# Optimization experiments

Hardware: AMD Instinct MI355X
Metric: run time of the kernel (lower is better)

Reference implementation:

```python
import jax, jax.numpy as jnp
import numpy as np

N = 50000        # nodes
E = 800000       # edges per meta-path (avg degree 16)
M = 3            # meta-paths
IN = 256         # in_size
HID = 16         # hidden_size (per-head out dim of GATConv)
HEADS = 8
OUT = 8          # out_size (classes)
SA_HID = 128     # StructureAttention hidden_size default
NEG_SLOPE = 0.2  # DGL GATConv leaky_relu default


def setup_inputs() -> dict:
    key = jax.random.key(0)
    ks = jax.random.split(key, 11)
    h = jax.random.normal(ks[0], (N, IN), jnp.float32)
    edges = jax.random.randint(ks[1], (M, 2, E), 0, N, jnp.int32)  # [M, (src,dst), E]
    s = 0.05
    fc_w = jax.random.normal(ks[2], (M, IN, HEADS * HID), jnp.float32) * s
    attn_l = jax.random.normal(ks[3], (M, HEADS, HID), jnp.float32) * s
    attn_r = jax.random.normal(ks[4], (M, HEADS, HID), jnp.float32) * s
    sa_w1 = jax.random.normal(ks[5], (HEADS * HID, SA_HID), jnp.float32) * s
    sa_b1 = jnp.zeros((SA_HID,), jnp.float32)
    sa_w2 = jax.random.normal(ks[6], (SA_HID, 1), jnp.float32) * s
    pred_w = jax.random.normal(ks[7], (HEADS * HID, OUT), jnp.float32) * s
    pred_b = jnp.zeros((OUT,), jnp.float32)
    return {"h": h, "edges": edges, "fc_w": fc_w, "attn_l": attn_l,
            "attn_r": attn_r, "sa_w1": sa_w1, "sa_b1": sa_b1, "sa_w2": sa_w2,
            "pred_w": pred_w, "pred_b": pred_b}


def _gat(h, src, dst, w, al, ar):
    # DGL GATConv, eval mode (dropout=0), activation=elu
    feat = (h @ w).reshape(N, HEADS, HID)                 # [N,H,D]
    el = jnp.einsum('nhd,hd->nh', feat, al)               # [N,H]
    er = jnp.einsum('nhd,hd->nh', feat, ar)               # [N,H]
    e = el[src] + er[dst]                                 # [E,H]
    e = jnp.where(e > 0, e, NEG_SLOPE * e)                # leaky_relu
    # edge softmax over incoming edges of each dst node
    emax = jax.ops.segment_max(e, dst, num_segments=N)    # [N,H]
    ex = jnp.exp(e - emax[dst])                           # [E,H]
    denom = jax.ops.segment_sum(ex, dst, num_segments=N)  # [N,H]
    alpha = ex / denom[dst]                               # [E,H]
    msg = feat[src] * alpha[:, :, None]                   # [E,H,D]
    out = jax.ops.segment_sum(msg, dst, num_segments=N)   # [N,H,D]
    return jax.nn.elu(out).reshape(N, HEADS * HID)        # flatten(1)


def reference(h, edges, fc_w, attn_l, attn_r, sa_w1, sa_b1, sa_w2, pred_w, pred_b):
    # per-meta-path GAT (loop over fixed small set of meta-paths)
    zs = [_gat(h, edges[i, 0], edges[i, 1], fc_w[i], attn_l[i], attn_r[i])
          for i in range(M)]
    z = jnp.stack(zs, axis=1)                             # [N, M, H*D]
    # StructureAttention exactly as in source: softmax over dim 0 (nodes)
    w = jnp.tanh(z @ sa_w1 + sa_b1) @ sa_w2               # [N, M, 1]
    beta = jax.nn.softmax(w, axis=0)                      # softmax over nodes
    fused = (beta * z).sum(0)                             # [M, H*D]
    return fused @ pred_w + pred_b                        # [M, OUT]
```

## Files before the change

### kernel.cpp

```cpp
#include <hip/hip_runtime.h>

#define N_NODES 50000
#define N_EDGES 800000
#define N_META 3
#define IN_DIM 256
#define HD 128
#define HEADS 8
#define HID 16
#define OUT_DIM 8
#define NBKT 196
#define BCAP 5120
#define TILE_E 4096
#define NUMPAD 2064
#define GEMM_BX ((N_NODES + 63) / 64)
#define ELER_BX ((N_NODES * HEADS + 255) / 256)

using bf16x8 = __attribute__((ext_vector_type(8))) short;
using f32x4  = __attribute__((ext_vector_type(4))) float;

__device__ __forceinline__ float bf2f(unsigned short u) {
  union { unsigned int i; float f; } x; x.i = ((unsigned int)u) << 16; return x.f;
}
__device__ __forceinline__ unsigned short f2bf(float f) {
  union { float f; unsigned int i; } x; x.f = f;
  unsigned int r = x.i + 0x7fffu + ((x.i >> 16) & 1u);
  return (unsigned short)(r >> 16);
}

__global__ __launch_bounds__(256)
void prep_kernel(const float* __restrict__ fcw, const float* __restrict__ w1,
                 unsigned short* __restrict__ fcwT, unsigned short* __restrict__ w1T) {
  int i = blockIdx.x * 256 + threadIdx.x;
  const int NFC = N_META * IN_DIM * HD;
  if (i < NFC) {
    int p = i / (IN_DIM * HD);
    int rem = i - p * (IN_DIM * HD);
    int k = rem / HD, n = rem - k * HD;
    fcwT[(size_t)p * HD * IN_DIM + n * IN_DIM + k] = f2bf(fcw[i]);
  } else if (i < NFC + HD * HD) {
    int j = i - NFC;
    int k = j / HD, n = j - k * HD;
    w1T[n * HD + k] = f2bf(w1[j]);
  }
}

__global__ __launch_bounds__(256)
void bin_gemm_kernel(const int* __restrict__ edges, int* __restrict__ gcur,
                     unsigned int* __restrict__ bktbuf,
                     const float* __restrict__ A,
                     const unsigned short* __restrict__ BT,
                     unsigned short* __restrict__ Cb, int nrows) {
  __shared__ char smem[15360];
  int p = blockIdx.y;
  int t = threadIdx.x;
  if (blockIdx.x < NBKT) {
    int* hist  = (int*)smem;
    int* gbase = hist + NBKT;
    int* fill  = gbase + NBKT;
    int e0 = blockIdx.x * TILE_E;
    const int* src = edges + (size_t)p * 2 * N_EDGES;
    const int* dst = src + N_EDGES;
    for (int i = t; i < NBKT; i += 256) { hist[i] = 0; fill[i] = 0; }
    __syncthreads();
    for (int i = t; i < TILE_E; i += 256) {
      int e = e0 + i;
      if (e < N_EDGES) atomicAdd(&hist[dst[e] >> 8], 1);
    }
    __syncthreads();
    for (int i = t; i < NBKT; i += 256) {
      int idx = p * NBKT + i;
      gbase[i] = hist[i] ? (idx * BCAP + atomicAdd(&gcur[idx], hist[i])) : 0;
    }
    __syncthreads();
    for (int i = t; i < TILE_E; i += 256) {
      int e = e0 + i;
      if (e < N_EDGES) {
        int d = dst[e];
        int b = d >> 8;
        int r = atomicAdd(&fill[b], 1);
        bktbuf[gbase[b] + r] = ((unsigned int)(d & 255) << 16) | (unsigned int)src[e];
      }
    }
  } else {
    unsigned short* As = (unsigned short*)smem;
    unsigned short* Bs = As + 64 * 40;
    int w = t >> 6, l = t & 63, q = l >> 4, s = l & 15;
    int row0 = (blockIdx.x - NBKT) * 64;
    const unsigned short* BTm = BT + (size_t)p * HD * IN_DIM;
    f32x4 acc[8] = {};
    for (int k0 = 0; k0 < IN_DIM; k0 += 32) {
      {
        int r = t >> 2, c = (t & 3) * 8;
        int gr = row0 + r;
        float4 a0, a1;
        if (gr < nrows) {
          a0 = *(const float4*)(A + (size_t)gr * IN_DIM + k0 + c);
          a1 = *(const float4*)(A + (size_t)gr * IN_DIM + k0 + c + 4);
        } else {
          a0 = make_float4(0.f, 0.f, 0.f, 0.f); a1 = a0;
        }
        ushort4 u0, u1;
        u0.x = f2bf(a0.x); u0.y = f2bf(a0.y); u0.z = f2bf(a0.z); u0.w = f2bf(a0.w);
        u1.x = f2bf(a1.x); u1.y = f2bf(a1.y); u1.z = f2bf(a1.z); u1.w = f2bf(a1.w);
        *(ushort4*)&As[r * 40 + c]     = u0;
        *(ushort4*)&As[r * 40 + c + 4] = u1;
      }
      {
        int n = t >> 1, c = (t & 1) * 16;
        uint4 b0 = *(const uint4*)(BTm + (size_t)n * IN_DIM + k0 + c);
        uint4 b1 = *(const uint4*)(BTm + (size_t)n * IN_DIM + k0 + c + 8);
        *(uint4*)&Bs[n * 40 + c]     = b0;
        *(uint4*)&Bs[n * 40 + c + 8] = b1;
      }
      __syncthreads();
      bf16x8 af = *(bf16x8*)&As[(w * 16 + s) * 40 + q * 8];
      #pragma unroll
      for (int f = 0; f < 8; ++f) {
        bf16x8 bf = *(bf16x8*)&Bs[(f * 16 + s) * 40 + q * 8];
        acc[f] = __builtin_amdgcn_mfma_f32_16x16x32_bf16(af, bf, acc[f], 0, 0, 0);
      }
      __syncthreads();
    }
    unsigned short* Cm = Cb + (size_t)p * N_NODES * HD;
    #pragma unroll
    for (int f = 0; f < 8; ++f) {
      #pragma unroll
      for (int r = 0; r < 4; ++r) {
        int gr = row0 + w * 16 + q * 4 + r;
        if (gr < nrows) Cm[(size_t)gr * HD + f * 16 + s] = f2bf(acc[f][r]);
      }
    }
  }
}

__global__ __launch_bounds__(256)
void sort_eler_kernel(const int* __restrict__ gcur,
                      const unsigned int* __restrict__ bktbuf,
                      int* __restrict__ offsB, int* __restrict__ offsE,
                      int* __restrict__ csr,
                      const unsigned short* __restrict__ featb3,
                      const float* __restrict__ al, const float* __restrict__ ar,
                      float* __restrict__ el3, float* __restrict__ er3) {
  __shared__ int lh[256];
  __shared__ int cur[256];
  __shared__ int wsum[4];
  int p = blockIdx.y;
  int t = threadIdx.x;
  if (blockIdx.x < NBKT) {
    int b = blockIdx.x;
    int lane = t & 63, wid = t >> 6;
    int idx = p * NBKT + b;
    int S = idx * BCAP;
    int E = S + gcur[idx];
    int node0 = b * 256;
    int nn = min(256, N_NODES - node0);
    int gi0 = p * N_NODES + node0;
    lh[t] = 0;
    __syncthreads();
    for (int i = S + t; i < E; i += 256) atomicAdd(&lh[bktbuf[i] >> 16], 1);
    __syncthreads();
    int v = lh[t];
    int s = v;
    #pragma unroll
    for (int d = 1; d < 64; d <<= 1) {
      int x = __shfl_up(s, d);
      if (lane >= d) s += x;
    }
    if (lane == 63) wsum[wid] = s;
    __syncthreads();
    int woff = 0;
    #pragma unroll
    for (int k = 0; k < 4; ++k) if (k < wid) woff += wsum[k];
    int excl = S + woff + s - v;
    if (t < nn) {
      offsB[gi0 + t] = excl;
      offsE[gi0 + t] = excl + v;
    }
    cur[t] = excl;
    __syncthreads();
    for (int i = S + t; i < E; i += 256) {
      unsigned int rec = bktbuf[i];
      int pos = atomicAdd(&cur[rec >> 16], 1);
      csr[pos] = (int)(rec & 0xffffu);
    }
  } else {
    int i = (blockIdx.x - NBKT) * 256 + t;
    if (i >= N_NODES * HEADS) return;
    int node = i >> 3, hh = i & 7;
    const unsigned short* f =
        featb3 + (size_t)p * N_NODES * HD + (size_t)node * HD + hh * HID;
    uint4 u0 = *(const uint4*)(f);
    uint4 u1 = *(const uint4*)(f + 8);
    unsigned int uu[8] = {u0.x, u0.y, u0.z, u0.w, u1.x, u1.y, u1.z, u1.w};
    const float* alm = al + p * HD + hh * HID;
    const float* arm = ar + p * HD + hh * HID;
    float sl = 0.f, sr = 0.f;
    #pragma unroll
    for (int q = 0; q < 8; ++q) {
      float v0 = __uint_as_float(uu[q] << 16);
      float v1 = __uint_as_float(uu[q] & 0xffff0000u);
      int d = q * 2;
      sl += v0 * alm[d] + v1 * alm[d + 1];
      sr += v0 * arm[d] + v1 * arm[d + 1];
    }
    el3[(size_t)p * N_NODES * HEADS + i] = sl;
    er3[(size_t)p * N_NODES * HEADS + i] = sr;
  }
}

__global__ __launch_bounds__(256)
void aggregate_kernel(const int* __restrict__ offsB3, const int* __restrict__ offsE3,
                      const int* __restrict__ csr,
                      const uint4* __restrict__ featb3_u4,
                      const float* __restrict__ el3, const float* __restrict__ er3,
                      uint4* __restrict__ zb3_u4) {
  int m = blockIdx.y;
  int node = blockIdx.x * 4 + (threadIdx.x >> 6);
  if (node >= N_NODES) return;
  const uint4* featb_u4 = featb3_u4 + (size_t)m * N_NODES * 16;
  const float* el = el3 + (size_t)m * N_NODES * HEADS;
  const float* er = er3 + (size_t)m * N_NODES * HEADS;
  uint4* z_u4 = zb3_u4 + (size_t)m * N_NODES * 16;
  int lane = threadIdx.x & 63;
  int k = lane >> 3, h = lane & 7;
  int qg = lane >> 4;
  int li = lane & 15;
  int ch = li >> 1;
  int beg = offsB3[m * N_NODES + node], end = offsE3[m * N_NODES + node];
  float erh = er[node * HEADS + h];
  float ssum = 0.f;
  float a[8] = {};
  int i = beg;
  for (; i + 8 <= end; i += 8) {
    int sl = csr[i + k];
    float e = el[sl * HEADS + h] + erh;
    e = e > 0.f ? e : 0.2f * e;
    float ev = __expf(e);
    ssum += ev;
    #pragma unroll
    for (int half = 0; half < 2; ++half) {
      int slot = half * 4 + qg;
      float wv = __shfl(ev, slot * 8 + ch);
      int sk = __shfl(sl, slot * 8);
      uint4 v = featb_u4[(size_t)sk * 16 + li];
      a[0] += wv * __uint_as_float(v.x << 16);
      a[1] += wv * __uint_as_float(v.x & 0xffff0000u);
      a[2] += wv * __uint_as_float(v.y << 16);
      a[3] += wv * __uint_as_float(v.y & 0xffff0000u);
      a[4] += wv * __uint_as_float(v.z << 16);
      a[5] += wv * __uint_as_float(v.z & 0xffff0000u);
      a[6] += wv * __uint_as_float(v.w << 16);
      a[7] += wv * __uint_as_float(v.w & 0xffff0000u);
    }
  }
  if (i < end) {
    int nk = end - i;
    int sl = 0; float ev = 0.f;
    if (k < nk) {
      sl = csr[i + k];
      float e = el[sl * HEADS + h] + erh;
      e = e > 0.f ? e : 0.2f * e;
      ev = __expf(e);
    }
    ssum += ev;
    #pragma unroll
    for (int half = 0; half < 2; ++half) {
      if (half * 4 < nk) {
        int slot = half * 4 + qg;
        float wv = __shfl(ev, slot * 8 + ch);
        int sk = __shfl(sl, slot * 8);
        uint4 v = featb_u4[(size_t)sk * 16 + li];
        a[0] += wv * __uint_as_float(v.x << 16);
        a[1] += wv * __uint_as_float(v.x & 0xffff0000u);
        a[2] += wv * __uint_as_float(v.y << 16);
        a[3] += wv * __uint_as_float(v.y & 0xffff0000u);
        a[4] += wv * __uint_as_float(v.z << 16);
        a[5] += wv * __uint_as_float(v.z & 0xffff0000u);
        a[6] += wv * __uint_as_float(v.w << 16);
        a[7] += wv * __uint_as_float(v.w & 0xffff0000u);
      }
    }
  }
  ssum += __shfl_xor(ssum, 8);
  ssum += __shfl_xor(ssum, 16);
  ssum += __shfl_xor(ssum, 32);
  float st = __shfl(ssum, ch);
  #pragma unroll
  for (int j = 0; j < 8; ++j) {
    a[j] += __shfl_xor(a[j], 16);
    a[j] += __shfl_xor(a[j], 32);
  }
  float inv = (end > beg) ? 1.f / st : 0.f;
  if (qg == 0) {
    uint4 o;
    unsigned int p0, p1;
    #pragma unroll
    for (int j = 0; j < 8; ++j) {
      float z = a[j] * inv;
      z = z > 0.f ? z : expm1f(z);
      a[j] = z;
    }
    p0 = (unsigned int)f2bf(a[0]) | ((unsigned int)f2bf(a[1]) << 16); o.x = p0;
    p1 = (unsigned int)f2bf(a[2]) | ((unsigned int)f2bf(a[3]) << 16); o.y = p1;
    p0 = (unsigned int)f2bf(a[4]) | ((unsigned int)f2bf(a[5]) << 16); o.z = p0;
    p1 = (unsigned int)f2bf(a[6]) | ((unsigned int)f2bf(a[7]) << 16); o.w = p1;
    z_u4[(size_t)node * 16 + li] = o;
  }
}

__global__ __launch_bounds__(256)
void w_gemm_mfma(const unsigned short* __restrict__ Zb3,
                 const unsigned short* __restrict__ BT,
                 const float* __restrict__ B1, const float* __restrict__ W2,
                 float* __restrict__ numpad3, int nrows) {
  __shared__ unsigned short Bs[128 * 136];
  __shared__ unsigned short As[64 * 136];
  __shared__ float wrow[64];
  __shared__ float part[4][64][2];
  __shared__ float dpart[4];
  int tid = threadIdx.x;
  int m = blockIdx.y;
  const unsigned short* Zb = Zb3 + (size_t)m * N_NODES * HD;
  float* numpad = numpad3 + (size_t)m * NUMPAD;
  int w = tid >> 6, l = tid & 63, q = l >> 4, s = l & 15;
  {
    int n = tid >> 1, c0 = (tid & 1) * 64;
    #pragma unroll
    for (int j = 0; j < 8; ++j)
      *(uint4*)&Bs[n * 136 + c0 + j * 8] = *(const uint4*)(BT + n * HD + c0 + j * 8);
  }
  float b1v[8], w2v[8];
  #pragma unroll
  for (int f = 0; f < 8; ++f) { b1v[f] = B1[f * 16 + s]; w2v[f] = W2[f * 16 + s]; }
  const unsigned int* Zu = (const unsigned int*)Zb;
  float a0 = 0.f, a1 = 0.f, ld = 0.f;
  for (int t = 0; t < 4; ++t) {
    int row0 = blockIdx.x * 256 + t * 64;
    __syncthreads();
    {
      int r = tid >> 2, c0 = (tid & 3) * 32;
      int gr = row0 + r;
      if (gr < nrows) {
        #pragma unroll
        for (int j = 0; j < 4; ++j)
          *(uint4*)&As[r * 136 + c0 + j * 8] =
              *(const uint4*)(Zb + (size_t)gr * HD + c0 + j * 8);
      } else {
        uint4 z = make_uint4(0, 0, 0, 0);
        #pragma unroll
        for (int j = 0; j < 4; ++j) *(uint4*)&As[r * 136 + c0 + j * 8] = z;
      }
    }
    __syncthreads();
    f32x4 acc[8] = {};
    #pragma unroll
    for (int kc = 0; kc < 4; ++kc) {
      bf16x8 af = *(bf16x8*)&As[(w * 16 + s) * 136 + kc * 32 + q * 8];
      #pragma unroll
      for (int f = 0; f < 8; ++f) {
        bf16x8 bf = *(bf16x8*)&Bs[(f * 16 + s) * 136 + kc * 32 + q * 8];
        acc[f] = __builtin_amdgcn_mfma_f32_16x16x32_bf16(af, bf, acc[f], 0, 0, 0);
      }
    }
    #pragma unroll
    for (int r = 0; r < 4; ++r) {
      float p = 0.f;
      #pragma unroll
      for (int f = 0; f < 8; ++f) p += tanhf(acc[f][r] + b1v[f]) * w2v[f];
      p += __shfl_xor(p, 1); p += __shfl_xor(p, 2);
      p += __shfl_xor(p, 4); p += __shfl_xor(p, 8);
      if (s == 0) wrow[w * 16 + q * 4 + r] = p;
    }
    __syncthreads();
    for (int r = w; r < 64; r += 4) {
      int gr = row0 + r;
      if (gr < nrows) {
        float e = __expf(wrow[r]);
        unsigned int v = Zu[(size_t)gr * 64 + l];
        a0 += e * __uint_as_float(v << 16);
        a1 += e * __uint_as_float(v & 0xffff0000u);
        if (l == 0) ld += e;
      }
    }
  }
  part[w][l][0] = a0;
  part[w][l][1] = a1;
  if (l == 0) dpart[w] = ld;
  __syncthreads();
  if (w == 0) {
    float s0 = part[0][l][0] + part[1][l][0] + part[2][l][0] + part[3][l][0];
    float s1 = part[0][l][1] + part[1][l][1] + part[2][l][1] + part[3][l][1];
    atomicAdd(&numpad[(2 * l) * 16], s0);
    atomicAdd(&numpad[(2 * l + 1) * 16], s1);
    if (l == 0)
      atomicAdd(&numpad[128 * 16], dpart[0] + dpart[1] + dpart[2] + dpart[3]);
  }
}

__global__ void final_kernel(const float* __restrict__ numpad,
                             const float* __restrict__ PW, const float* __restrict__ PB,
                             float* __restrict__ out) {
  int t = threadIdx.x;
  if (t >= N_META * OUT_DIM) return;
  int m = t >> 3, o = t & 7;
  const float* np = numpad + m * NUMPAD;
  float inv = 1.0f / np[128 * 16];
  float s = 0.f;
  for (int k = 0; k < HD; ++k) s += np[k * 16] * PW[k * OUT_DIM + o];
  out[t] = s * inv + PB[o];
}

extern "C" void kernel_launch(void* const* d_in, const int* in_sizes, int n_in,
                              void* d_out, int out_size, void* d_ws, size_t ws_size,
                              hipStream_t stream) {
  (void)in_sizes; (void)n_in; (void)out_size; (void)ws_size;
  const float* h     = (const float*)d_in[0];
  const int*   edges = (const int*)d_in[1];
  const float* fcw   = (const float*)d_in[2];
  const float* al    = (const float*)d_in[3];
  const float* ar    = (const float*)d_in[4];
  const float* w1    = (const float*)d_in[5];
  const float* b1    = (const float*)d_in[6];
  const float* w2    = (const float*)d_in[7];
  const float* pw    = (const float*)d_in[8];
  const float* pb    = (const float*)d_in[9];
  float* out = (float*)d_out;

  char* ws = (char*)d_ws;
  size_t off = 0;
  auto alloc = [&](size_t bytes) -> void* {
    void* p = ws + off;
    off = (off + bytes + 255) & ~(size_t)255;
    return p;
  };
  unsigned short* featb3 = (unsigned short*)alloc((size_t)N_META * N_NODES * HD * 2);
  unsigned short* zb3    = (unsigned short*)alloc((size_t)N_META * N_NODES * HD * 2);
  unsigned short* fcwT   = (unsigned short*)alloc((size_t)N_META * HD * IN_DIM * 2);
  unsigned short* w1T    = (unsigned short*)alloc((size_t)HD * HD * 2);
  float* el3 = (float*)alloc((size_t)N_META * N_NODES * HEADS * 4);
  float* er3 = (float*)alloc((size_t)N_META * N_NODES * HEADS * 4);
  int* gcur  = (int*)alloc((size_t)N_META * NBKT * 4);
  int* offsB = (int*)alloc((size_t)N_META * N_NODES * 4);
  int* offsE = (int*)alloc((size_t)N_META * N_NODES * 4);
  unsigned int* bktbuf = (unsigned int*)alloc((size_t)N_META * NBKT * BCAP * 4);
  int* csr   = (int*)alloc((size_t)N_META * NBKT * BCAP * 4);
  float* numpad = (float*)alloc((size_t)N_META * NUMPAD * 4);

  hipMemsetAsync(numpad, 0, (size_t)N_META * NUMPAD * 4, stream);
  hipMemsetAsync(gcur, 0, (size_t)N_META * NBKT * 4, stream);

  prep_kernel<<<(N_META * IN_DIM * HD + HD * HD + 255) / 256, 256, 0, stream>>>(
      fcw, w1, fcwT, w1T);

  dim3 agrid_(NBKT + GEMM_BX, N_META);
  bin_gemm_kernel<<<agrid_, 256, 0, stream>>>(
      edges, gcur, bktbuf, h, fcwT, featb3, N_NODES);

  dim3 bgrid_(NBKT + ELER_BX, N_META);
  sort_eler_kernel<<<bgrid_, 256, 0, stream>>>(
      gcur, bktbuf, offsB, offsE, csr, featb3, al, ar, el3, er3);

  dim3 ggrid((N_NODES + 3) / 4, N_META);
  aggregate_kernel<<<ggrid, 256, 0, stream>>>(
      offsB, offsE, csr, (const uint4*)featb3, el3, er3, (uint4*)zb3);

  dim3 wgrid((N_NODES + 255) / 256, N_META);
  w_gemm_mfma<<<wgrid, 256, 0, stream>>>(zb3, w1T, b1, w2, numpad, N_NODES);

  final_kernel<<<1, 64, 0, stream>>>(numpad, pw, pb, out);
}
```

Baseline: 366.6 us.

## Pre-convert h to bf16, split aggregate per meta-path, use fast tanh

Result: slower. 390.1 us (+6.4%).

```diff
diff --git a/kernel.cpp b/kernel.cpp
--- a/kernel.cpp
+++ b/kernel.cpp
@@ -14,6 +14,8 @@
 #define NUMPAD 2064
 #define GEMM_BX ((N_NODES + 63) / 64)
 #define ELER_BX ((N_NODES * HEADS + 255) / 256)
+#define PREP_BX 448
+#define H2B_BX  6250
 
 using bf16x8 = __attribute__((ext_vector_type(8))) short;
 using f32x4  = __attribute__((ext_vector_type(4))) float;
@@ -26,28 +28,46 @@
   unsigned int r = x.i + 0x7fffu + ((x.i >> 16) & 1u);
   return (unsigned short)(r >> 16);
 }
+__device__ __forceinline__ float tanh_fast(float x) {
+  float e = __expf(2.f * x);
+  return 1.f - 2.f / (e + 1.f);
+}
 
 __global__ __launch_bounds__(256)
 void prep_kernel(const float* __restrict__ fcw, const float* __restrict__ w1,
-                 unsigned short* __restrict__ fcwT, unsigned short* __restrict__ w1T) {
-  int i = blockIdx.x * 256 + threadIdx.x;
-  const int NFC = N_META * IN_DIM * HD;
-  if (i < NFC) {
-    int p = i / (IN_DIM * HD);
-    int rem = i - p * (IN_DIM * HD);
-    int k = rem / HD, n = rem - k * HD;
-    fcwT[(size_t)p * HD * IN_DIM + n * IN_DIM + k] = f2bf(fcw[i]);
-  } else if (i < NFC + HD * HD) {
-    int j = i - NFC;
-    int k = j / HD, n = j - k * HD;
-    w1T[n * HD + k] = f2bf(w1[j]);
+                 const float* __restrict__ h,
+                 unsigned short* __restrict__ fcwT, unsigned short* __restrict__ w1T,
+                 unsigned short* __restrict__ hb) {
+  if (blockIdx.x < PREP_BX) {
+    int i = blockIdx.x * 256 + threadIdx.x;
+    const int NFC = N_META * IN_DIM * HD;
+    if (i < NFC) {
+      int p = i / (IN_DIM * HD);
+      int rem = i - p * (IN_DIM * HD);
+      int k = rem / HD, n = rem - k * HD;
+      fcwT[(size_t)p * HD * IN_DIM + n * IN_DIM + k] = f2bf(fcw[i]);
+    } else if (i < NFC + HD * HD) {
+      int j = i - NFC;
+      int k = j / HD, n = j - k * HD;
+      w1T[n * HD + k] = f2bf(w1[j]);
+    }
+  } else {
+    size_t j = (size_t)(blockIdx.x - PREP_BX) * 256 + threadIdx.x;
+    size_t base = j * 8;
+    float4 a0 = *(const float4*)(h + base);
+    float4 a1 = *(const float4*)(h + base + 4);
+    ushort4 u0, u1;
+    u0.x = f2bf(a0.x); u0.y = f2bf(a0.y); u0.z = f2bf(a0.z); u0.w = f2bf(a0.w);
+    u1.x = f2bf(a1.x); u1.y = f2bf(a1.y); u1.z = f2bf(a1.z); u1.w = f2bf(a1.w);
+    *(ushort4*)(hb + base)     = u0;
+    *(ushort4*)(hb + base + 4) = u1;
   }
 }
 
 __global__ __launch_bounds__(256)
 void bin_gemm_kernel(const int* __restrict__ edges, int* __restrict__ gcur,
                      unsigned int* __restrict__ bktbuf,
-                     const float* __restrict__ A,
+                     const unsigned short* __restrict__ HB,
                      const unsigned short* __restrict__ BT,
                      unsigned short* __restrict__ Cb, int nrows) {
   __shared__ char smem[15360];
@@ -92,18 +112,9 @@
       {
         int r = t >> 2, c = (t & 3) * 8;
         int gr = row0 + r;
-        float4 a0, a1;
-        if (gr < nrows) {
-          a0 = *(const float4*)(A + (size_t)gr * IN_DIM + k0 + c);
-          a1 = *(const float4*)(A + (size_t)gr * IN_DIM + k0 + c + 4);
-        } else {
-          a0 = make_float4(0.f, 0.f, 0.f, 0.f); a1 = a0;
-        }
-        ushort4 u0, u1;
-        u0.x = f2bf(a0.x); u0.y = f2bf(a0.y); u0.z = f2bf(a0.z); u0.w = f2bf(a0.w);
-        u1.x = f2bf(a1.x); u1.y = f2bf(a1.y); u1.z = f2bf(a1.z); u1.w = f2bf(a1.w);
-        *(ushort4*)&As[r * 40 + c]     = u0;
-        *(ushort4*)&As[r * 40 + c + 4] = u1;
+        uint4 a = make_uint4(0, 0, 0, 0);
+        if (gr < nrows) a = *(const uint4*)(HB + (size_t)gr * IN_DIM + k0 + c);
+        *(uint4*)&As[r * 40 + c] = a;
       }
       {
         int n = t >> 1, c = (t & 1) * 16;
@@ -213,8 +224,7 @@
                       const int* __restrict__ csr,
                       const uint4* __restrict__ featb3_u4,
                       const float* __restrict__ el3, const float* __restrict__ er3,
-                      uint4* __restrict__ zb3_u4) {
-  int m = blockIdx.y;
+                      uint4* __restrict__ zb3_u4, int m) {
   int node = blockIdx.x * 4 + (threadIdx.x >> 6);
   if (node >= N_NODES) return;
   const uint4* featb_u4 = featb3_u4 + (size_t)m * N_NODES * 16;
@@ -366,7 +376,7 @@
     for (int r = 0; r < 4; ++r) {
       float p = 0.f;
       #pragma unroll
-      for (int f = 0; f < 8; ++f) p += tanhf(acc[f][r] + b1v[f]) * w2v[f];
+      for (int f = 0; f < 8; ++f) p += tanh_fast(acc[f][r] + b1v[f]) * w2v[f];
       p += __shfl_xor(p, 1); p += __shfl_xor(p, 2);
       p += __shfl_xor(p, 4); p += __shfl_xor(p, 8);
       if (s == 0) wrow[w * 16 + q * 4 + r] = p;
@@ -433,6 +443,7 @@
     off = (off + bytes + 255) & ~(size_t)255;
     return p;
   };
+  unsigned short* hb     = (unsigned short*)alloc((size_t)N_NODES * IN_DIM * 2);
   unsigned short* featb3 = (unsigned short*)alloc((size_t)N_META * N_NODES * HD * 2);
   unsigned short* zb3    = (unsigned short*)alloc((size_t)N_META * N_NODES * HD * 2);
   unsigned short* fcwT   = (unsigned short*)alloc((size_t)N_META * HD * IN_DIM * 2);
@@ -449,20 +460,19 @@
   hipMemsetAsync(numpad, 0, (size_t)N_META * NUMPAD * 4, stream);
   hipMemsetAsync(gcur, 0, (size_t)N_META * NBKT * 4, stream);
 
-  prep_kernel<<<(N_META * IN_DIM * HD + HD * HD + 255) / 256, 256, 0, stream>>>(
-      fcw, w1, fcwT, w1T);
+  prep_kernel<<<PREP_BX + H2B_BX, 256, 0, stream>>>(fcw, w1, h, fcwT, w1T, hb);
 
   dim3 agrid_(NBKT + GEMM_BX, N_META);
   bin_gemm_kernel<<<agrid_, 256, 0, stream>>>(
-      edges, gcur, bktbuf, h, fcwT, featb3, N_NODES);
+      edges, gcur, bktbuf, hb, fcwT, featb3, N_NODES);
 
   dim3 bgrid_(NBKT + ELER_BX, N_META);
   sort_eler_kernel<<<bgrid_, 256, 0, stream>>>(
       gcur, bktbuf, offsB, offsE, csr, featb3, al, ar, el3, er3);
 
-  dim3 ggrid((N_NODES + 3) / 4, N_META);
-  aggregate_kernel<<<ggrid, 256, 0, stream>>>(
-      offsB, offsE, csr, (const uint4*)featb3, el3, er3, (uint4*)zb3);
+  for (int m = 0; m < N_META; ++m)
+    aggregate_kernel<<<(N_NODES + 3) / 4, 256, 0, stream>>>(
+        offsB, offsE, csr, (const uint4*)featb3, el3, er3, (uint4*)zb3, m);
 
   dim3 wgrid((N_NODES + 255) / 256, N_META);
   w_gemm_mfma<<<wgrid, 256, 0, stream>>>(zb3, w1T, b1, w2, numpad, N_NODES);
```
